# Kernel tuning notes

Hardware: AMD Instinct MI355X
Metric: run time of the kernel (lower is better)

## Reference

```python
import jax, jax.numpy as jnp
import numpy as np

B_, T_, N_ = 32, 96, 68
IN_F, HID, GRU_H, NCLS = 3, 128, 128, 10
DEG = 8
N_NODES = B_ * T_ * N_
N_EDGES = N_NODES * DEG


def setup_inputs() -> dict:
    key = jax.random.key(0)
    ks = jax.random.split(key, 16)
    s = 0.05
    rn = lambda k, shp: (jax.random.normal(k, shp, jnp.float32) * s)
    return {
        "x": jax.random.normal(ks[0], (N_NODES, IN_F), jnp.float32),
        "edge_index": jax.random.randint(ks[1], (2, N_EDGES), 0, N_NODES, jnp.int32),
        "W_gcn0": rn(ks[2], (IN_F, HID)),
        "b_gcn0": jnp.zeros((HID,), jnp.float32),
        "W_gcn1": rn(ks[3], (HID, HID)),
        "b_gcn1": jnp.zeros((HID,), jnp.float32),
        "W_mlp": rn(ks[4], (HID, HID)),
        "b_mlp": jnp.zeros((HID,), jnp.float32),
        "W_ih": rn(ks[5], (3 * GRU_H, HID)),
        "W_hh": rn(ks[6], (3 * GRU_H, GRU_H)),
        "b_ih": jnp.zeros((3 * GRU_H,), jnp.float32),
        "b_hh": jnp.zeros((3 * GRU_H,), jnp.float32),
        "W_c1": rn(ks[7], (GRU_H, GRU_H // 2)),
        "b_c1": jnp.zeros((GRU_H // 2,), jnp.float32),
        "W_c2": rn(ks[8], (GRU_H // 2, NCLS)),
        "b_c2": jnp.zeros((NCLS,), jnp.float32),
        "B": B_, "T": T_, "N": N_,
    }


def reference(x, edge_index, W_gcn0, b_gcn0, W_gcn1, b_gcn1, W_mlp, b_mlp,
              W_ih, W_hh, b_ih, b_hh, W_c1, b_c1, W_c2, b_c2, B, T, N):
    n_nodes = x.shape[0]
    src, dst = edge_index[0], edge_index[1]
    # GCN degree with self-loops: deg[i] = 1 + in-degree(i)
    deg = jnp.ones((n_nodes,), x.dtype).at[dst].add(1.0)
    d_isqrt = jax.lax.rsqrt(deg)
    self_norm = (d_isqrt * d_isqrt)[:, None]  # self-loop norm = 1/deg
    edge_norm = (d_isqrt[src] * d_isqrt[dst])[:, None]

    def gcn(h, W, b):
        h = h @ W
        agg = jax.ops.segment_sum(h[src] * edge_norm, dst, num_segments=n_nodes)
        return agg + h * self_norm + b

    h = jax.nn.relu(gcn(x, W_gcn0, b_gcn0))
    h = jax.nn.relu(gcn(h, W_gcn1, b_gcn1))
    h = jax.nn.relu(h @ W_mlp + b_mlp)  # node_mlp (dropout off in eval)

    frames = h.reshape(B, T, N, -1).mean(axis=2)  # [B, T, HID] frame pooling

    def gru_step(hs, xt):
        gi = xt @ W_ih.T + b_ih
        gh = hs @ W_hh.T + b_hh
        ir, iz, inn = jnp.split(gi, 3, axis=-1)
        hr, hz, hn = jnp.split(gh, 3, axis=-1)
        r = jax.nn.sigmoid(ir + hr)
        z = jax.nn.sigmoid(iz + hz)
        n_new = jnp.tanh(inn + r * hn)
        return (1.0 - z) * n_new + z * hs, None

    h0 = jnp.zeros((B, GRU_H), frames.dtype)
    hT, _ = jax.lax.scan(gru_step, h0, jnp.swapaxes(frames, 0, 1))

    hidden = jax.nn.relu(hT @ W_c1 + b_c1)
    return hidden @ W_c2 + b_c2  # logits [B, num_classes]
```

## Files before the change

kernel.cpp:

```cpp
#include <hip/hip_runtime.h>

#define NN_TOT 208896
#define E_TOT  1671168
#define B_SZ   32
#define T_SZ   96
#define NPF    68
#define HID    128
#define NBINS  204
#define CAP    9216
#define NSB    816

typedef _Float16 f16x8 __attribute__((ext_vector_type(8)));
typedef _Float16 f16x2v __attribute__((ext_vector_type(2)));
typedef float f32x4 __attribute__((ext_vector_type(4)));

__global__ __launch_bounds__(256) void k_scatter(const int* __restrict__ src, const int* __restrict__ dst,
                                                 int* __restrict__ gcur, int* __restrict__ er_tmp,
                                                 const float* __restrict__ Wih, const float* __restrict__ Whh,
                                                 const float* __restrict__ W1, const float* __restrict__ Wm,
                                                 const float* __restrict__ W0, const float* __restrict__ b0,
                                                 _Float16* __restrict__ Wihh, _Float16* __restrict__ Wihl,
                                                 _Float16* __restrict__ W1p, _Float16* __restrict__ Wmp,
                                                 _Float16* __restrict__ Whhp, _Float16* __restrict__ W0h,
                                                 _Float16* __restrict__ b0h) {
    const int bid = blockIdx.x;
    const int tid = threadIdx.x;
    if (bid >= NSB) {
        int i = (bid - NSB) * 256 + tid;
        {
            int e = i & 7;
            int lane = (i >> 3) & 63;
            int f = i >> 9;
            int j = f >> 2, kk = f & 3;
            int q = lane >> 4, p = lane & 15;
            float wv = Wih[(size_t)(j * 16 + p) * 128 + kk * 32 + q * 8 + e];
            _Float16 hi = (_Float16)wv;
            Wihh[i] = hi;
            Wihl[i] = (_Float16)(wv - (float)hi);
        }
        {
            int e = i & 7;
            int lane = (i >> 3) & 63;
            int f = i >> 9;
            int kk = f & 3, g = (f >> 2) % 3, wv = f / 12;
            int q = lane >> 4, c = lane & 15;
            Whhp[i] = (_Float16)Whh[(size_t)(g * 128 + 16 * wv + c) * 128 + kk * 32 + q * 8 + e];
        }
        if (i < 16384) {
            int f = i >> 9;
            int j = f >> 2, kk = f & 3;
            int lane = (i >> 3) & 63;
            int e = i & 7;
            int q = lane >> 4, p = lane & 15;
            int k = kk * 32 + q * 8 + e, n = j * 16 + p;
            W1p[i] = (_Float16)W1[k * 128 + n];
            Wmp[i] = (_Float16)Wm[k * 128 + n];
        }
        if (i < 384) W0h[i] = (_Float16)W0[i];
        if (i < 128) b0h[i] = (_Float16)b0[i];
        return;
    }
    __shared__ int hist[NBINS];
    __shared__ int lbase[NBINS];
    for (int i = tid; i < NBINS; i += 256) hist[i] = 0;
    __syncthreads();
    const int be = bid * 2048 + tid * 8;
    int s[8], d[8], rk[8];
    *(int4*)&s[0] = *(const int4*)&src[be];
    *(int4*)&s[4] = *(const int4*)&src[be + 4];
    *(int4*)&d[0] = *(const int4*)&dst[be];
    *(int4*)&d[4] = *(const int4*)&dst[be + 4];
#pragma unroll
    for (int j = 0; j < 8; ++j) rk[j] = atomicAdd(&hist[d[j] >> 10], 1);
    __syncthreads();
    for (int i = tid; i < NBINS; i += 256) lbase[i] = atomicAdd(&gcur[i], hist[i]);
    __syncthreads();
#pragma unroll
    for (int j = 0; j < 8; ++j) {
        int b = d[j] >> 10;
        er_tmp[(size_t)b * CAP + lbase[b] + rk[j]] = s[j] | ((d[j] & 1023) << 18);
    }
}

__global__ __launch_bounds__(256) void k_binsort2(const int* __restrict__ er_tmp, const int* __restrict__ gcur,
                                                  const float* __restrict__ x, int* __restrict__ er,
                                                  int2* __restrict__ row2, float4* __restrict__ xd) {
    __shared__ int lcnt[1024];
    __shared__ int lofs[1024];
    __shared__ int ts[256];
    const int tid = threadIdx.x;
    const int nb = blockIdx.x << 10;
    const int base0 = blockIdx.x * CAP;
    for (int i = tid; i < 1024; i += 256) lcnt[i] = 0;
    __syncthreads();
    const int nrec = gcur[blockIdx.x];
    int rec[36];
#pragma unroll
    for (int j = 0; j < 36; ++j) {
        int idx = tid + j * 256;
        rec[j] = (idx < nrec) ? er_tmp[base0 + idx] : -1;
    }
#pragma unroll
    for (int j = 0; j < 36; ++j)
        if (rec[j] >= 0) atomicAdd(&lcnt[rec[j] >> 18], 1);
    __syncthreads();
    const int base = tid * 4;
    const int c0 = lcnt[base], c1 = lcnt[base + 1], c2 = lcnt[base + 2], c3 = lcnt[base + 3];
    int ssum = c0 + c1 + c2 + c3;
    ts[tid] = ssum;
    __syncthreads();
    int inc = ssum;
    for (int off = 1; off < 256; off <<= 1) {
        int add = (tid >= off) ? ts[tid - off] : 0;
        __syncthreads();
        inc += add;
        ts[tid] = inc;
        __syncthreads();
    }
    const int b0 = base0 + (inc - ssum);
    lofs[base] = b0;
    lofs[base + 1] = b0 + c0;
    lofs[base + 2] = b0 + c0 + c1;
    lofs[base + 3] = b0 + c0 + c1 + c2;
    row2[nb + base] = make_int2(b0, b0 + c0);
    row2[nb + base + 1] = make_int2(b0 + c0, b0 + c0 + c1);
    row2[nb + base + 2] = make_int2(b0 + c0 + c1, b0 + c0 + c1 + c2);
    row2[nb + base + 3] = make_int2(b0 + c0 + c1 + c2, b0 + ssum);
    {
        const float4* xv = (const float4*)(x + 3 * (size_t)(nb + base));
        float4 a = xv[0], b = xv[1], c = xv[2];
        float i0 = 1.0f / sqrtf(1.f + (float)c0);
        float i1 = 1.0f / sqrtf(1.f + (float)c1);
        float i2 = 1.0f / sqrtf(1.f + (float)c2);
        float i3 = 1.0f / sqrtf(1.f + (float)c3);
        xd[nb + base + 0] = make_float4(a.x * i0, a.y * i0, a.z * i0, i0);
        xd[nb + base + 1] = make_float4(a.w * i1, b.x * i1, b.y * i1, i1);
        xd[nb + base + 2] = make_float4(b.z * i2, b.w * i2, c.x * i2, i2);
        xd[nb + base + 3] = make_float4(c.y * i3, c.z * i3, c.w * i3, i3);
    }
    __syncthreads();
#pragma unroll
    for (int j = 0; j < 36; ++j)
        if (rec[j] >= 0) {
            int p = atomicAdd(&lofs[rec[j] >> 18], 1);
            er[p] = rec[j] & 0x3FFFF;
        }
}

__global__ __launch_bounds__(256) void k_z0(const float4* __restrict__ xd, const int2* __restrict__ row2,
                                            const int* __restrict__ er, float4* __restrict__ z0out) {
    const int tid = threadIdx.x;
    const int blk = blockIdx.x;
    const int li = tid >> 2;
    const int slot = tid & 3;
    const int n = blk * 64 + li;
    const int2 be2 = row2[n];
    float p0 = 0.f, p1 = 0.f, p2 = 0.f;
    for (int ei = be2.x + slot; ei < be2.y; ei += 4) {
        float4 f = xd[er[ei]];
        p0 += f.x;
        p1 += f.y;
        p2 += f.z;
    }
    p0 += __shfl_xor(p0, 1); p1 += __shfl_xor(p1, 1); p2 += __shfl_xor(p2, 1);
    p0 += __shfl_xor(p0, 2); p1 += __shfl_xor(p1, 2); p2 += __shfl_xor(p2, 2);
    if (slot == 0) {
        const float4 own = xd[n];
        const float w = own.w;
        float4 z;
        z.x = w * (p0 + own.x);
        z.y = w * (p1 + own.y);
        z.z = w * (p2 + own.z);
        z.w = w;
        z0out[n] = z;
    }
}

__global__ __launch_bounds__(256, 4) void k_agg_mm(const float4* __restrict__ z0, const int2* __restrict__ row2,
                                                   const int* __restrict__ er, const _Float16* __restrict__ W0h,
                                                   const _Float16* __restrict__ b0h, const _Float16* __restrict__ W1p,
                                                   const float* __restrict__ b1, const _Float16* __restrict__ Wmp,
                                                   const float* __restrict__ bm, float* __restrict__ fr32) {
    __shared__ __align__(16) _Float16 As[64 * 136];
    __shared__ __align__(16) _Float16 Bs[64 * 136];
    __shared__ float colpart[4 * 2 * 128];
    const int tid = threadIdx.x;
    const int w = tid >> 6, lane = tid & 63;
    const int blk = blockIdx.x;

    {
        const int node = blk * 64 + lane;
        const int2 be2 = row2[node];
        const int beg = be2.x, end = be2.y;
        int ei = beg;
        int sa_c = 0, sb_c = 0, sa_n = 0, sb_n = 0;
        float4 za_c, zb_c;
        if (ei + 2 <= end) { sa_c = er[ei]; sb_c = er[ei + 1]; }
        if (ei + 4 <= end) { sa_n = er[ei + 2]; sb_n = er[ei + 3]; }
        const float4 zs = z0[node];
        if (ei + 2 <= end) { za_c = z0[sa_c]; zb_c = z0[sb_c]; }

        const f16x2v* __restrict__ W0p = (const f16x2v*)W0h;
        const f16x2v* __restrict__ b0p = (const f16x2v*)b0h;
        const int pb = w * 16;
        const f16x2v zero2 = {(_Float16)0.f, (_Float16)0.f};
        f16x2v w0p[16], w1p[16], w2p[16], bbp[16];
#pragma unroll
        for (int j = 0; j < 16; ++j) {
            w0p[j] = W0p[pb + j];
            w1p[j] = W0p[64 + pb + j];
            w2p[j] = W0p[128 + pb + j];
            bbp[j] = b0p[pb + j];
        }
        const _Float16 isd = (_Float16)zs.w;
        const f16x2v dnn = {isd, isd};
        f16x2v accp[16];
        {
            _Float16 sx = (_Float16)zs.x, sy = (_Float16)zs.y, sz = (_Float16)zs.z;
            f16x2v zxx = {sx, sx}, zyy = {sy, sy}, zzz = {sz, sz};
#pragma unroll
            for (int j = 0; j < 16; ++j) {
                f16x2v t = zxx * w0p[j] + (zyy * w1p[j] + (zzz * w2p[j] + bbp[j]));
                t = __builtin_elementwise_max(t, zero2);
                accp[j] = t * dnn;
            }
        }
        for (; ei + 2 <= end; ei += 2) {
            float4 za_nv, zb_nv;
            int sa_nn = 0, sb_nn = 0;
            if (ei + 4 <= end) { za_nv = z0[sa_n]; zb_nv = z0[sb_n]; }
            if (ei + 6 <= end) { sa_nn = er[ei + 4]; sb_nn = er[ei + 5]; }
            const float4 za = za_c, zb = zb_c;
            _Float16 ax = (_Float16)za.x, ay = (_Float16)za.y, az = (_Float16)za.z;
            _Float16 aen = (_Float16)za.w;
            _Float16 bx = (_Float16)zb.x, by = (_Float16)zb.y, bz = (_Float16)zb.z;
            _Float16 ben = (_Float16)zb.w;
            f16x2v axx = {ax, ax}, ayy = {ay, ay}, azz = {az, az}, aee = {aen, aen};
            f16x2v bxx = {bx, bx}, byy = {by, by}, bzz = {bz, bz}, bee = {ben, ben};
#pragma unroll
            for (int j = 0; j < 16; ++j) {
                f16x2v t = axx * w0p[j] + (ayy * w1p[j] + (azz * w2p[j] + bbp[j]));
                t = __builtin_elementwise_max(t, zero2);
                accp[j] = t * aee + accp[j];
            }
#pragma unroll
            for (int j = 0; j < 16; ++j) {
                f16x2v t = bxx * w0p[j] + (byy * w1p[j] + (bzz * w2p[j] + bbp[j]));
                t = __builtin_elementwise_max(t, zero2);
                accp[j] = t * bee + accp[j];
            }
            za_c = za_nv; zb_c = zb_nv;
            sa_n = sa_nn; sb_n = sb_nn;
        }
        if (ei < end) {
            float4 za = z0[er[ei]];
            _Float16 ax = (_Float16)za.x, ay = (_Float16)za.y, az = (_Float16)za.z;
            _Float16 aen = (_Float16)za.w;
            f16x2v axx = {ax, ax}, ayy = {ay, ay}, azz = {az, az}, aee = {aen, aen};
#pragma unroll
            for (int j = 0; j < 16; ++j) {
                f16x2v t = axx * w0p[j] + (ayy * w1p[j] + (azz * w2p[j] + bbp[j]));
                t = __builtin_elementwise_max(t, zero2);
                accp[j] = t * aee + accp[j];
            }
        }
        _Float16* dst = &As[lane * 136 + w * 32];
#pragma unroll
        for (int j = 0; j < 16; ++j) *(f16x2v*)(dst + 2 * j) = accp[j] * dnn;
    }
    __syncthreads();

    const int q = lane >> 4, c = lane & 15;
    {
        f16x8 afr[4];
#pragma unroll
        for (int kk = 0; kk < 4; ++kk) afr[kk] = *(const f16x8*)(&As[(w * 16 + c) * 136 + kk * 32 + q * 8]);
        const f16x8* __restrict__ Bv = (const f16x8*)W1p;
#pragma unroll
        for (int j = 0; j < 8; ++j) {
            f32x4 cc = {0.f, 0.f, 0.f, 0.f};
#pragma unroll
            for (int kk = 0; kk < 4; ++kk)
                cc = __builtin_amdgcn_mfma_f32_16x16x32_f16(afr[kk], Bv[(j * 4 + kk) * 64 + lane], cc, 0, 0, 0);
            const float bi = b1[j * 16 + c];
#pragma unroll
            for (int r = 0; r < 4; ++r)
                Bs[(w * 16 + q * 4 + r) * 136 + j * 16 + c] = (_Float16)fmaxf(cc[r] + bi, 0.f);
        }
    }

    {
        f16x8 afr2[4];
#pragma unroll
        for (int kk = 0; kk < 4; ++kk) afr2[kk] = *(const f16x8*)(&Bs[(w * 16 + c) * 136 + kk * 32 + q * 8]);
        const f16x8* __restrict__ Bv2 = (const f16x8*)Wmp;
        const int f0 = (blk * 64) / NPF;
        const int cut = (f0 + 1) * NPF;
        const int rowg0 = blk * 64 + w * 16 + q * 4;
#pragma unroll
        for (int j = 0; j < 8; ++j) {
            f32x4 cc = {0.f, 0.f, 0.f, 0.f};
#pragma unroll
            for (int kk = 0; kk < 4; ++kk)
                cc = __builtin_amdgcn_mfma_f32_16x16x32_f16(afr2[kk], Bv2[(j * 4 + kk) * 64 + lane], cc, 0, 0, 0);
            const float bi = bm[j * 16 + c];
            float sA = 0.f, sB = 0.f;
#pragma unroll
            for (int r = 0; r < 4; ++r) {
                float v = fmaxf(cc[r] + bi, 0.f);
                if (rowg0 + r < cut) sA += v; else sB += v;
            }
            sA += __shfl_xor(sA, 16);
            sA += __shfl_xor(sA, 32);
            sB += __shfl_xor(sB, 16);
            sB += __shfl_xor(sB, 32);
            if (lane < 16) {
                colpart[(w * 2 + 0) * 128 + j * 16 + c] = sA;
                colpart[(w * 2 + 1) * 128 + j * 16 + c] = sB;
            }
        }
    }
    __syncthreads();
    {
        const int f = tid >> 7, col = tid & 127;
        float s = colpart[(0 * 2 + f) * 128 + col] + colpart[(1 * 2 + f) * 128 + col] +
                  colpart[(2 * 2 + f) * 128 + col] + colpart[(3 * 2 + f) * 128 + col];
        const int f0 = (blk * 64) / NPF;
        if (f == 0) {
            atomicAdd(&fr32[(size_t)f0 * 128 + col], s);
        } else {
            const int f1 = (blk * 64 + 63) / NPF;
            if (f1 != f0) atomicAdd(&fr32[(size_t)f1 * 128 + col], s);
        }
    }
}

__global__ __launch_bounds__(256) void k_gi(const float* __restrict__ fr32,
                                            const _Float16* __restrict__ Wihh, const _Float16* __restrict__ Wihl,
                                            const float* __restrict__ bih, const float* __restrict__ bhh,
                                            float* __restrict__ GIt) {
    __shared__ __align__(16) _Float16 Ah[64 * 136];
    __shared__ __align__(16) _Float16 Al[64 * 136];
    const int tid = threadIdx.x;
    const int w = tid >> 6, lane = tid & 63;
    const int q = lane >> 4, p = lane & 15;
    const int nb = blockIdx.x * 64;

    for (int idx = tid; idx < 64 * 128; idx += 256) {
        int row = idx >> 7, col = idx & 127;
        float v = fr32[(size_t)(nb + row) * 128 + col] * (1.0f / NPF);
        _Float16 hi = (_Float16)v;
        Ah[row * 136 + col] = hi;
        Al[row * 136 + col] = (_Float16)(v - (float)hi);
    }
    __syncthreads();

    f16x8 ah[4], al[4];
#pragma unroll
    for (int kk = 0; kk < 4; ++kk) {
        ah[kk] = *(const f16x8*)(&Ah[(w * 16 + p) * 136 + kk * 32 + q * 8]);
        al[kk] = *(const f16x8*)(&Al[(w * 16 + p) * 136 + kk * 32 + q * 8]);
    }
    const f16x8* __restrict__ Bh = (const f16x8*)Wihh;
    const f16x8* __restrict__ Bl = (const f16x8*)Wihl;
    int dr[4];
#pragma unroll
    for (int r = 0; r < 4; ++r) {
        int m = nb + w * 16 + q * 4 + r;
        int bb = m / 96, tt = m - bb * 96;
        dr[r] = (tt * B_SZ + bb) * 384;
    }
#pragma unroll
    for (int j = 0; j < 24; ++j) {
        f32x4 cc = {0.f, 0.f, 0.f, 0.f};
#pragma unroll
        for (int kk = 0; kk < 4; ++kk)
            cc = __builtin_amdgcn_mfma_f32_16x16x32_f16(ah[kk], Bh[(j * 4 + kk) * 64 + lane], cc, 0, 0, 0);
#pragma unroll
        for (int kk = 0; kk < 4; ++kk)
            cc = __builtin_amdgcn_mfma_f32_16x16x32_f16(ah[kk], Bl[(j * 4 + kk) * 64 + lane], cc, 0, 0, 0);
#pragma unroll
        for (int kk = 0; kk < 4; ++kk)
            cc = __builtin_amdgcn_mfma_f32_16x16x32_f16(al[kk], Bh[(j * 4 + kk) * 64 + lane], cc, 0, 0, 0);
        const int o = j * 16 + p;
        const float bias = bih[o] + ((o < 256) ? bhh[o] : 0.f);
        const float scale = (o < 256) ? -1.44269504f : 1.f;
#pragma unroll
        for (int r = 0; r < 4; ++r) GIt[dr[r] + o] = (cc[r] + bias) * scale;
    }
}

#define GRU_SYNC()                                              \
    asm volatile("s_waitcnt lgkmcnt(0)" ::: "memory");          \
    __builtin_amdgcn_s_barrier();                               \
    __builtin_amdgcn_sched_barrier(0);

#define GRU_BODY(PAR, GU, GL, JOFF)                                                                  \
    {                                                                                                \
        const _Float16* rb = hbuf[PAR];                                                              \
        _Float16* wb = hbuf[PAR ^ 1];                                                                \
        f16x8 afr[4];                                                                                \
        _Pragma("unroll") for (int kk = 0; kk < 4; ++kk)                                             \
            afr[kk] = *(const f16x8*)(&rb[c * 144 + kk * 32 + q * 8]);                               \
        const float* lp = pb + (size_t)(JOFF + 2) * STRIDE;                                          \
        _Pragma("unroll") for (int r = 0; r < 4; ++r)                                                \
            _Pragma("unroll") for (int g = 0; g < 3; ++g)                                            \
                GL[r * 3 + g] = lp[r * 384 + g * 128];                                               \
        f32x4 cc[3];                                                                                 \
        _Pragma("unroll") for (int g = 0; g < 3; ++g) {                                              \
            f32x4 a = {0.f, 0.f, 0.f, 0.f};                                                          \
            _Pragma("unroll") for (int kk = 0; kk < 4; ++kk)                                         \
                a = __builtin_amdgcn_mfma_f32_16x16x32_f16(afr[kk], bfr[g][kk], a, 0, 0, 0);         \
            cc[g] = a;                                                                               \
        }                                                                                            \
        _Pragma("unroll") for (int r = 0; r < 4; ++r) {                                              \
            float hn = cc[2][r] + bh2;                                                               \
            float rg = __builtin_amdgcn_rcpf(1.f + exp2f(fmaf(mL2E, cc[0][r], GU[r * 3 + 0])));      \
            float zg = __builtin_amdgcn_rcpf(1.f + exp2f(fmaf(mL2E, cc[1][r], GU[r * 3 + 1])));      \
            float arg = fmaf(rg, hn, GU[r * 3 + 2]);                                                 \
            float u = __builtin_amdgcn_rcpf(exp2f(2.f * L2E * arg) + 1.f);                           \
            float nn = fmaf(-2.f, u, 1.f);                                                           \
            h[r] = fmaf(zg, h[r] - nn, nn);                                                          \
            if (q < 2) wb[(q * 4 + r) * 144 + 16 * w + c] = (_Float16)h[r];                          \
        }                                                                                            \
        GRU_SYNC()                                                                                   \
    }

__global__ __launch_bounds__(512) __attribute__((amdgpu_waves_per_eu(1, 2)))
void k_gru(const float* __restrict__ GIt, const _Float16* __restrict__ Whhp,
           const float* __restrict__ bhh,
           const float* __restrict__ Wc1, const float* __restrict__ bc1,
           const float* __restrict__ Wc2, const float* __restrict__ bc2,
           float* __restrict__ out, float* __restrict__ hst,
           int t0, int iters, int last) {
    __shared__ __align__(16) _Float16 hbuf[2][16 * 144];
    const int tid = threadIdx.x;
    const int w = tid >> 6, lane = tid & 63;
    const int q = lane >> 4, c = lane & 15;
    const int B = blockIdx.x;
    const float L2E = 1.44269504f;
    const float mL2E = -1.44269504f;
    const int STRIDE = B_SZ * 384;

    f16x8 bfr[3][4];
#pragma unroll
    for (int g = 0; g < 3; ++g)
#pragma unroll
        for (int kk = 0; kk < 4; ++kk)
            bfr[g][kk] = *(const f16x8*)(Whhp + (size_t)(((w * 3 + g) * 4 + kk) * 64 + lane) * 8);
    const float bh2 = bhh[256 + 16 * w + c];
    for (int i = tid; i < 2 * 16 * 144 / 2; i += 512) ((unsigned int*)hbuf)[i] = 0u;
    float h[4] = {0.f, 0.f, 0.f, 0.f};

    const int qq = (q < 2) ? q : 1;
    if (t0 != 0) {
#pragma unroll
        for (int r = 0; r < 4; ++r) h[r] = hst[(size_t)(B * 8 + qq * 4 + r) * 128 + 16 * w + c];
    }
    const float* pb = GIt + (size_t)t0 * STRIDE + (size_t)(B * 8 + qq * 4) * 384 + 16 * w + c;
    float g0[12], g1[12], g2[12];
#pragma unroll
    for (int r = 0; r < 4; ++r)
#pragma unroll
        for (int g = 0; g < 3; ++g) {
            g0[r * 3 + g] = pb[r * 384 + g * 128];
            g1[r * 3 + g] = pb[STRIDE + r * 384 + g * 128];
        }
    __syncthreads();
    if (t0 != 0 && q < 2) {
#pragma unroll
        for (int r = 0; r < 4; ++r) hbuf[0][(q * 4 + r) * 144 + 16 * w + c] = (_Float16)h[r];
    }
    GRU_SYNC()

    for (int it = 0; it < iters; ++it) {
        GRU_BODY(0, g0, g2, 0)
        GRU_BODY(1, g1, g0, 1)
        GRU_BODY(0, g2, g1, 2)
        GRU_BODY(1, g0, g2, 3)
        GRU_BODY(0, g1, g0, 4)
        GRU_BODY(1, g2, g1, 5)
        pb += 6 * (size_t)STRIDE;
    }

    if (!last) {
        if (q < 2) {
#pragma unroll
            for (int r = 0; r < 4; ++r) hst[(size_t)(B * 8 + q * 4 + r) * 128 + 16 * w + c] = h[r];
        }
        return;
    }

    float* hbf = (float*)hbuf;
    float* hid = hbf + 1024;
    __syncthreads();
    if (q < 2) {
#pragma unroll
        for (int r = 0; r < 4; ++r) hbf[(q * 4 + r) * 128 + 16 * w + c] = h[r];
    }
    __syncthreads();
    {
        const int b = tid >> 6, j = tid & 63;
        const float* hb = hbf + b * 128;
        float a0 = bc1[j], a1 = 0.f, a2 = 0.f, a3 = 0.f;
#pragma unroll
        for (int k = 0; k < 128; k += 4) {
            a0 = fmaf(hb[k], Wc1[k * 64 + j], a0);
            a1 = fmaf(hb[k + 1], Wc1[(k + 1) * 64 + j], a1);
            a2 = fmaf(hb[k + 2], Wc1[(k + 2) * 64 + j], a2);
            a3 = fmaf(hb[k + 3], Wc1[(k + 3) * 64 + j], a3);
        }
        hid[tid] = fmaxf((a0 + a1) + (a2 + a3), 0.f);
    }
    __syncthreads();
    if (tid < 80) {
        int b = tid / 10, cc2 = tid % 10;
        float a = bc2[cc2];
#pragma unroll 8
        for (int k = 0; k < 64; ++k) a = fmaf(hid[b * 64 + k], Wc2[k * 10 + cc2], a);
        out[(B * 8 + b) * 10 + cc2] = a;
    }
}

extern "C" void kernel_launch(void* const* d_in, const int* in_sizes, int n_in, void* d_out, int out_size, void* d_ws,
                              size_t ws_size, hipStream_t stream) {
    const float* x = (const float*)d_in[0];
    const int* ei = (const int*)d_in[1];
    const int* e_src = ei;
    const int* e_dst = ei + E_TOT;
    const float* W0 = (const float*)d_in[2];
    const float* b0 = (const float*)d_in[3];
    const float* W1 = (const float*)d_in[4];
    const float* b1 = (const float*)d_in[5];
    const float* Wm = (const float*)d_in[6];
    const float* bm = (const float*)d_in[7];
    const float* Wih = (const float*)d_in[8];
    const float* Whh = (const float*)d_in[9];
    const float* bih = (const float*)d_in[10];
    const float* bhh = (const float*)d_in[11];
    const float* Wc1 = (const float*)d_in[12];
    const float* bc1 = (const float*)d_in[13];
    const float* Wc2 = (const float*)d_in[14];
    const float* bc2 = (const float*)d_in[15];
    float* out = (float*)d_out;

    char* base = (char*)d_ws;
    size_t off = 0;
    auto alloc = [&](size_t bytes) {
        size_t o = off;
        off = (off + bytes + 255) & ~(size_t)255;
        return o;
    };
    size_t o_gcur = alloc(256 * 4);
    size_t o_row2 = alloc((size_t)NN_TOT * 8);
    size_t o_er = alloc((size_t)NBINS * CAP * 4);
    size_t o_ertmp = alloc((size_t)NBINS * CAP * 4);
    size_t o_xd = alloc((size_t)NN_TOT * 16);
    size_t o_fr32 = alloc((size_t)B_SZ * T_SZ * 128 * 4);
    size_t o_gi = alloc((size_t)(T_SZ + 2) * B_SZ * 384 * 4);
    size_t o_hst = alloc((size_t)B_SZ * 128 * 4);
    size_t o_wihh = alloc((size_t)384 * 128 * 2);
    size_t o_wihl = alloc((size_t)384 * 128 * 2);
    size_t o_w1p = alloc((size_t)128 * 128 * 2);
    size_t o_wmp = alloc((size_t)128 * 128 * 2);
    size_t o_whhp = alloc((size_t)128 * 384 * 2);
    size_t o_w0h = alloc((size_t)384 * 2);
    size_t o_b0h = alloc((size_t)128 * 2);
    size_t o_z0 = alloc((size_t)NN_TOT * 16);
    if (off > ws_size) return;

    int* gcur = (int*)(base + o_gcur);
    int2* row2 = (int2*)(base + o_row2);
    int* er = (int*)(base + o_er);
    int* er_tmp = (int*)(base + o_ertmp);
    float4* xd = (float4*)(base + o_xd);
    float* fr32 = (float*)(base + o_fr32);
    float* GIt = (float*)(base + o_gi);
    float* hst = (float*)(base + o_hst);
    _Float16* Wihh = (_Float16*)(base + o_wihh);
    _Float16* Wihl = (_Float16*)(base + o_wihl);
    _Float16* W1p = (_Float16*)(base + o_w1p);
    _Float16* Wmp = (_Float16*)(base + o_wmp);
    _Float16* Whhp = (_Float16*)(base + o_whhp);
    _Float16* W0h = (_Float16*)(base + o_w0h);
    _Float16* b0h = (_Float16*)(base + o_b0h);
    float4* z0 = (float4*)(base + o_z0);

    hipMemsetAsync(base + o_gcur, 0, 256 * 4, stream);
    hipMemsetAsync(base + o_fr32, 0, (size_t)B_SZ * T_SZ * 128 * 4, stream);

    k_scatter<<<NSB + 192, 256, 0, stream>>>(e_src, e_dst, gcur, er_tmp,
                                             Wih, Whh, W1, Wm, W0, b0,
                                             Wihh, Wihl, W1p, Wmp, Whhp, W0h, b0h);
    k_binsort2<<<NBINS, 256, 0, stream>>>(er_tmp, gcur, x, er, row2, xd);
    k_z0<<<NN_TOT / 64, 256, 0, stream>>>(xd, row2, er, z0);
    k_agg_mm<<<NN_TOT / 64, 256, 0, stream>>>(z0, row2, er, W0h, b0h, W1p, b1, Wmp, bm, fr32);
    k_gi<<<B_SZ * T_SZ / 64, 256, 0, stream>>>(fr32, Wihh, Wihl, bih, bhh, GIt);
    k_gru<<<4, 512, 0, stream>>>(GIt, Whhp, bhh, Wc1, bc1, Wc2, bc2, out, hst, 0, 5, 0);
    k_gru<<<4, 512, 0, stream>>>(GIt, Whhp, bhh, Wc1, bc1, Wc2, bc2, out, hst, 30, 5, 0);
    k_gru<<<4, 512, 0, stream>>>(GIt, Whhp, bhh, Wc1, bc1, Wc2, bc2, out, hst, 60, 6, 1);
}
```

Before: 352.7 us.

## Stage scatter records in LDS for grouped writes; split agg_mm into three launches

The edge scatter kernel now computes per-block bin offsets with a shared-memory prefix scan. It stages the records and their destinations in LDS, then writes them out in bin-sorted order so global stores to each bin land contiguously rather than scattered. This costs extra LDS (about 17 KB), several barriers and the scan. Separately, the aggregation+matmul kernel is split into three launches of 1088 blocks each via a block offset, which adds launch overhead and may change scheduling or cache behaviour.

Measured after the change: 370.0 us. 1.05x slower.

```diff
diff --git a/kernel.cpp b/kernel.cpp
--- a/kernel.cpp
+++ b/kernel.cpp
@@ -61,7 +61,11 @@
         return;
     }
     __shared__ int hist[NBINS];
+    __shared__ int lofs[NBINS];
     __shared__ int lbase[NBINS];
+    __shared__ int ts[256];
+    __shared__ int recs[2048];
+    __shared__ int dsta[2048];
     for (int i = tid; i < NBINS; i += 256) hist[i] = 0;
     __syncthreads();
     const int be = bid * 2048 + tid * 8;
@@ -73,12 +77,34 @@
 #pragma unroll
     for (int j = 0; j < 8; ++j) rk[j] = atomicAdd(&hist[d[j] >> 10], 1);
     __syncthreads();
+    {
+        int v = (tid < NBINS) ? hist[tid] : 0;
+        ts[tid] = v;
+        __syncthreads();
+        int inc = v;
+        for (int off = 1; off < 256; off <<= 1) {
+            int add = (tid >= off) ? ts[tid - off] : 0;
+            __syncthreads();
+            inc += add;
+            ts[tid] = inc;
+            __syncthreads();
+        }
+        if (tid < NBINS) lofs[tid] = inc - v;
+    }
     for (int i = tid; i < NBINS; i += 256) lbase[i] = atomicAdd(&gcur[i], hist[i]);
     __syncthreads();
 #pragma unroll
     for (int j = 0; j < 8; ++j) {
         int b = d[j] >> 10;
-        er_tmp[(size_t)b * CAP + lbase[b] + rk[j]] = s[j] | ((d[j] & 1023) << 18);
+        int pos = lofs[b] + rk[j];
+        recs[pos] = s[j] | ((d[j] & 1023) << 18);
+        dsta[pos] = b * CAP + lbase[b] + rk[j];
+    }
+    __syncthreads();
+#pragma unroll
+    for (int it = 0; it < 8; ++it) {
+        int p = tid + it * 256;
+        er_tmp[dsta[p]] = recs[p];
     }
 }
 
@@ -180,13 +206,13 @@
                                                    const int* __restrict__ er, const _Float16* __restrict__ W0h,
                                                    const _Float16* __restrict__ b0h, const _Float16* __restrict__ W1p,
                                                    const float* __restrict__ b1, const _Float16* __restrict__ Wmp,
-                                                   const float* __restrict__ bm, float* __restrict__ fr32) {
+                                                   const float* __restrict__ bm, float* __restrict__ fr32, int bofs) {
     __shared__ __align__(16) _Float16 As[64 * 136];
     __shared__ __align__(16) _Float16 Bs[64 * 136];
     __shared__ float colpart[4 * 2 * 128];
     const int tid = threadIdx.x;
     const int w = tid >> 6, lane = tid & 63;
-    const int blk = blockIdx.x;
+    const int blk = blockIdx.x + bofs;
 
     {
         const int node = blk * 64 + lane;
@@ -594,7 +620,9 @@
                                              Wihh, Wihl, W1p, Wmp, Whhp, W0h, b0h);
     k_binsort2<<<NBINS, 256, 0, stream>>>(er_tmp, gcur, x, er, row2, xd);
     k_z0<<<NN_TOT / 64, 256, 0, stream>>>(xd, row2, er, z0);
-    k_agg_mm<<<NN_TOT / 64, 256, 0, stream>>>(z0, row2, er, W0h, b0h, W1p, b1, Wmp, bm, fr32);
+    k_agg_mm<<<1088, 256, 0, stream>>>(z0, row2, er, W0h, b0h, W1p, b1, Wmp, bm, fr32, 0);
+    k_agg_mm<<<1088, 256, 0, stream>>>(z0, row2, er, W0h, b0h, W1p, b1, Wmp, bm, fr32, 1088);
+    k_agg_mm<<<1088, 256, 0, stream>>>(z0, row2, er, W0h, b0h, W1p, b1, Wmp, bm, fr32, 2176);
     k_gi<<<B_SZ * T_SZ / 64, 256, 0, stream>>>(fr32, Wihh, Wihl, bih, bhh, GIt);
     k_gru<<<4, 512, 0, stream>>>(GIt, Whhp, bhh, Wc1, bc1, Wc2, bc2, out, hst, 0, 5, 0);
     k_gru<<<4, 512, 0, stream>>>(GIt, Whhp, bhh, Wc1, bc1, Wc2, bc2, out, hst, 30, 5, 0);
```
